# Kernel tuning notes

Hardware: AMD Instinct MI355X
Metric: run time of the kernel (lower is better)

## Reference

```python
import jax, jax.numpy as jnp
import numpy as np

# Fixed MANO structural constants (from MANO_RIGHT.pkl)
PARENTS = np.array([-1, 0, 1, 2, 0, 4, 5, 0, 7, 8, 0, 10, 11, 0, 13, 14])
FINGERTIP = np.array([745, 333, 444, 555, 672])
REMAP = np.array([0, 13, 14, 15, 16, 1, 2, 3, 17, 4, 5, 6, 18, 10, 11, 12, 19, 7, 8, 9, 20])
NV, NJ, NB, NP = 778, 16, 10, 135  # verts, joints, shape betas, pose-basis dim


def setup_inputs() -> dict:
    key = jax.random.key(0)
    ks = jax.random.split(key, 9)
    B = 8192
    beta = jax.random.normal(ks[0], (B, NB), jnp.float32)
    pose = jax.random.normal(ks[1], (B, NJ - 1, 3), jnp.float32) * 0.3
    rvec = jax.random.normal(ks[2], (B, 3), jnp.float32) * 0.3
    tvec = jax.random.normal(ks[3], (B, 3), jnp.float32)
    V = jax.random.normal(ks[4], (NV, 3), jnp.float32) * 0.1          # v_template
    S = jax.random.normal(ks[5], (NV, 3, NB), jnp.float32) * 0.01     # shapedirs
    P = jax.random.normal(ks[6], (NP, NV * 3), jnp.float32) * 0.01    # posedirs (reshaped, transposed)
    J_reg = jax.random.uniform(ks[7], (NJ, NV), jnp.float32)
    J_reg = J_reg / jnp.sum(J_reg, axis=-1, keepdims=True)
    W = jax.random.uniform(ks[8], (NV, NJ), jnp.float32)
    W = W / jnp.sum(W, axis=-1, keepdims=True)                        # skinning weights
    return {"beta": beta, "pose": pose, "rvec": rvec, "tvec": tvec,
            "V": V, "S": S, "P": P, "J_reg": J_reg, "W": W}


def _rodrigues(r):
    # r: [..., 3] axis-angle -> [..., 3, 3] rotation matrices
    sq = jnp.sum(r * r, axis=-1, keepdims=True)
    angle = jnp.sqrt(sq + 1e-8)
    axis = r / angle
    cos = jnp.cos(angle)[..., None]
    sin = jnp.sin(angle)[..., None]
    x, y, z = axis[..., 0], axis[..., 1], axis[..., 2]
    zeros = jnp.zeros_like(x)
    K = jnp.stack([zeros, -z, y, z, zeros, -x, -y, x, zeros], axis=-1)
    K = K.reshape(r.shape[:-1] + (3, 3))
    outer = axis[..., :, None] * axis[..., None, :]
    eye = jnp.eye(3, dtype=r.dtype)
    return cos * eye + (1.0 - cos) * outer + sin * K


def reference(beta, pose, rvec, tvec, V, S, P, J_reg, W):
    B = beta.shape[0]
    dtype = beta.dtype
    full_pose = jnp.concatenate([rvec[:, None, :], pose], axis=1)          # [B,16,3]
    # shape blendshapes
    v_shaped = V + jnp.einsum('bl,vkl->bvk', beta, S)                      # [B,778,3]
    Jrest = jnp.einsum('jv,bvk->bjk', J_reg, v_shaped)                     # [B,16,3]
    # pose blendshapes
    rot = _rodrigues(full_pose)                                            # [B,16,3,3]
    pose_feat = (rot[:, 1:] - jnp.eye(3, dtype=dtype)).reshape(B, NP)      # [B,135]
    v_posed = v_shaped + jnp.matmul(pose_feat, P).reshape(B, NV, 3)        # [B,778,3]
    # rigid transforms along the kinematic chain
    rel = Jrest.at[:, 1:].add(-Jrest[:, PARENTS[1:]])                      # parent-relative joint offsets
    T = jnp.zeros((B, NJ, 4, 4), dtype=dtype)
    T = T.at[..., :3, :3].set(rot).at[..., :3, 3].set(rel).at[..., 3, 3].set(1.0)
    chain = [T[:, 0]]
    for i in range(1, NJ):
        chain.append(jnp.matmul(chain[int(PARENTS[i])], T[:, i]))
    A = jnp.stack(chain, axis=1)                                           # [B,16,4,4] world transforms
    posed_joints = A[..., :3, 3]                                           # [B,16,3]
    # relative-to-rest transforms: A_rel = A - pad(A @ [Jrest;0])
    corr = jnp.einsum('bjmn,bjn->bjm', A[..., :3, :3], Jrest)
    A_rel = A.at[..., :3, 3].add(-corr)
    # linear blend skinning
    Tv = jnp.einsum('vj,bjmn->bvmn', W, A_rel)                             # [B,778,4,4]
    verts = jnp.einsum('bvmn,bvn->bvm', Tv[..., :3, :3], v_posed) + Tv[..., :3, 3]
    # 16 joints + 5 fingertips, remapped to 21 joints
    joints = jnp.concatenate([posed_joints, verts[:, FINGERTIP]], axis=1)[:, REMAP]
    verts = verts + tvec[:, None, :]
    joints = joints + tvec[:, None, :]
    return verts, joints
```

## Files before the change

kernel.cpp:

```cpp
#include <hip/hip_runtime.h>
#include <hip/hip_bf16.h>

typedef __attribute__((ext_vector_type(8))) short short8v;
typedef __attribute__((ext_vector_type(4))) float float4v;

#define BATCH 8192
#define NVERT 778
#define NJOINT 16
#define NPOSE 135
#define KEXT  160
#define NVT   52

#define WSB_JS    0u
#define WSB_PFX   4096u
#define WSB_A     (WSB_PFX  + 2621440u)
#define WSB_PTXF  (WSB_A    + 6291456u)
#define WSB_WF    (WSB_PTXF + 798720u)
#define WSB_ATF   (WSB_WF   + 53248u)

__global__ __launch_bounds__(256) void js_kernel(
    const float* __restrict__ S, const float* __restrict__ V,
    const float* __restrict__ J_reg, float* __restrict__ wsJS)
{
    int o = blockIdx.x * 4 + (threadIdx.x >> 6);
    int lane = threadIdx.x & 63;
    float s = 0.f;
    if (o < 480) {
        int j = o / 30, k = (o / 10) % 3, l = o % 10;
        for (int v = lane; v < NVERT; v += 64)
            s += J_reg[j * NVERT + v] * S[v * 30 + k * 10 + l];
    } else if (o < 528) {
        int o2 = o - 480;
        int j = o2 / 3, k = o2 % 3;
        for (int v = lane; v < NVERT; v += 64)
            s += J_reg[j * NVERT + v] * V[v * 3 + k];
    }
#pragma unroll
    for (int m = 32; m >= 1; m >>= 1) s += __shfl_xor(s, m, 64);
    if (lane == 0 && o < 528) wsJS[o] = s;
}

__device__ __forceinline__ void rodrigues(float x, float y, float z, float R[9])
{
    float sq = x * x + y * y + z * z;
    float angle = sqrtf(sq + 1e-8f);
    float inv = 1.0f / angle;
    float ax = x * inv, ay = y * inv, az = z * inv;
    float c = cosf(angle), s = sinf(angle);
    float ic = 1.0f - c;
    R[0] = c + ic * ax * ax;      R[1] = ic * ax * ay - s * az; R[2] = ic * ax * az + s * ay;
    R[3] = ic * ax * ay + s * az; R[4] = c + ic * ay * ay;      R[5] = ic * ay * az - s * ax;
    R[6] = ic * ax * az - s * ay; R[7] = ic * ay * az + s * ax; R[8] = c + ic * az * az;
}

__device__ __forceinline__ void writeATF(
    __hip_bfloat16* __restrict__ ATF, int b, int i,
    const float R[9], const float t[3], const float J[3], const float tv[3])
{
    int bt = b >> 4;
    int lane32 = ((i >> 3) << 4) + (b & 15);
    size_t base = (((size_t)bt * 12) * 32 + lane32) * 8 + (i & 7);
    float vals[12];
#pragma unroll
    for (int m = 0; m < 3; ++m) {
        vals[m * 4 + 0] = R[m * 3 + 0];
        vals[m * 4 + 1] = R[m * 3 + 1];
        vals[m * 4 + 2] = R[m * 3 + 2];
        vals[m * 4 + 3] = t[m] + tv[m] - (R[m * 3 + 0] * J[0] + R[m * 3 + 1] * J[1] + R[m * 3 + 2] * J[2]);
    }
#pragma unroll
    for (int mn = 0; mn < 12; ++mn)
        ATF[base + (size_t)mn * 256] = __float2bfloat16(vals[mn]);
}

__global__ __launch_bounds__(256) void buildchain_kernel(
    const float* __restrict__ S, const float* __restrict__ V,
    const float* __restrict__ P, const float* __restrict__ W,
    const float* __restrict__ beta, const float* __restrict__ pose,
    const float* __restrict__ rvec, const float* __restrict__ tvec,
    const float* __restrict__ wsJS,
    __hip_bfloat16* __restrict__ PtxF, __hip_bfloat16* __restrict__ WF,
    __hip_bfloat16* __restrict__ pfx, __hip_bfloat16* __restrict__ ATF,
    float* __restrict__ out_joints)
{
    if (blockIdx.x < 208) {
        int idx = blockIdx.x * 256 + threadIdx.x;
        if (idx < NVT * 3 * 5 * 64) {
            int vt = idx / 960;
            int rem = idx % 960;
            int k = rem / 320;
            int rem2 = rem % 320;
            int kc = rem2 / 64;
            int lane = rem2 % 64;
            int v = vt * 16 + (lane & 15);
            int kbase = kc * 32 + (lane >> 4) * 8;
            short8v out;
#pragma unroll
            for (int jj = 0; jj < 8; ++jj) {
                int kk = kbase + jj;
                float val = 0.f;
                if (v < NVERT) {
                    if (kk < NPOSE)            val = P[(size_t)kk * (NVERT * 3) + v * 3 + k];
                    else if (kk < NPOSE + 10)  val = S[v * 30 + k * 10 + (kk - NPOSE)];
                    else if (kk == NPOSE + 10) val = V[v * 3 + k];
                }
                __hip_bfloat16 h = __float2bfloat16(val);
                out[jj] = *reinterpret_cast<short*>(&h);
            }
            ((short8v*)PtxF)[idx] = out;
        } else if (idx < NVT * 3 * 5 * 64 + NVT * 64) {
            int t = idx - NVT * 3 * 5 * 64;
            int vt = t / 64, lane = t % 64;
            int v = vt * 16 + (lane & 15);
            int jbase = (lane >> 4) * 8;
            short8v out;
#pragma unroll
            for (int jj = 0; jj < 8; ++jj) {
                int j = jbase + jj;
                float val = (j < 16 && v < NVERT) ? W[v * 16 + j] : 0.f;
                __hip_bfloat16 h = __float2bfloat16(val);
                out[jj] = *reinterpret_cast<short*>(&h);
            }
            ((short8v*)WF)[t] = out;
        }
        return;
    }

    int t = (blockIdx.x - 208) * 256 + threadIdx.x;
    int c = t >> 13;
    int b = t & (BATCH - 1);
    if (c >= 5) return;

    const int INVMAP[16] = {0, 5, 6, 7, 9, 10, 11, 17, 18, 19, 13, 14, 15, 1, 2, 3};

    float bt[10];
#pragma unroll
    for (int l = 0; l < 10; ++l) bt[l] = beta[b * 10 + l];

    float Jr0[3], Jrc[3][3];
#pragma unroll
    for (int k = 0; k < 3; ++k) {
        float s = wsJS[480 + k];
#pragma unroll
        for (int l = 0; l < 10; ++l) s += wsJS[k * 10 + l] * bt[l];
        Jr0[k] = s;
    }
#pragma unroll
    for (int sI = 0; sI < 3; ++sI) {
        int j = 3 * c + 1 + sI;
#pragma unroll
        for (int k = 0; k < 3; ++k) {
            float s = wsJS[480 + j * 3 + k];
#pragma unroll
            for (int l = 0; l < 10; ++l) s += wsJS[(j * 3 + k) * 10 + l] * bt[l];
            Jrc[sI][k] = s;
        }
    }

    float tv[3] = {tvec[b * 3 + 0], tvec[b * 3 + 1], tvec[b * 3 + 2]};

    float R0[9];
    rodrigues(rvec[b * 3 + 0], rvec[b * 3 + 1], rvec[b * 3 + 2], R0);
    float t0[3] = {Jr0[0], Jr0[1], Jr0[2]};

    __hip_bfloat16* pfb = pfx + (size_t)b * KEXT;
    float* jout = out_joints + (size_t)b * 63;

    if (c == 0) {
#pragma unroll
        for (int l = 0; l < 10; ++l) pfb[NPOSE + l] = __float2bfloat16(bt[l]);
        pfb[NPOSE + 10] = __float2bfloat16(1.0f);
#pragma unroll
        for (int l = NPOSE + 11; l < KEXT; ++l) pfb[l] = __float2bfloat16(0.0f);

#pragma unroll
        for (int k = 0; k < 3; ++k) jout[INVMAP[0] * 3 + k] = t0[k] + tv[k];
        writeATF(ATF, b, 0, R0, t0, Jr0, tv);
    }

    float Rc[9], tc[3], prevJ[3];
#pragma unroll
    for (int q = 0; q < 9; ++q) Rc[q] = R0[q];
#pragma unroll
    for (int k = 0; k < 3; ++k) { tc[k] = t0[k]; prevJ[k] = Jr0[k]; }

#pragma unroll
    for (int s = 0; s < 3; ++s) {
        int i = 3 * c + 1 + s;
        float Ri[9];
        rodrigues(pose[b * 45 + (i - 1) * 3 + 0],
                  pose[b * 45 + (i - 1) * 3 + 1],
                  pose[b * 45 + (i - 1) * 3 + 2], Ri);
#pragma unroll
        for (int mn = 0; mn < 9; ++mn)
            pfb[(i - 1) * 9 + mn] =
                __float2bfloat16(Ri[mn] - ((mn == 0 || mn == 4 || mn == 8) ? 1.0f : 0.0f));

        float rel[3];
#pragma unroll
        for (int k = 0; k < 3; ++k) rel[k] = Jrc[s][k] - prevJ[k];

        float Rn[9], tn[3];
#pragma unroll
        for (int m = 0; m < 3; ++m) {
#pragma unroll
            for (int n = 0; n < 3; ++n)
                Rn[m * 3 + n] = Rc[m * 3 + 0] * Ri[0 + n] + Rc[m * 3 + 1] * Ri[3 + n] + Rc[m * 3 + 2] * Ri[6 + n];
            tn[m] = Rc[m * 3 + 0] * rel[0] + Rc[m * 3 + 1] * rel[1] + Rc[m * 3 + 2] * rel[2] + tc[m];
        }
#pragma unroll
        for (int q = 0; q < 9; ++q) Rc[q] = Rn[q];
#pragma unroll
        for (int k = 0; k < 3; ++k) { tc[k] = tn[k]; prevJ[k] = Jrc[s][k]; }

#pragma unroll
        for (int k = 0; k < 3; ++k) jout[INVMAP[i] * 3 + k] = tc[k] + tv[k];

        writeATF(ATF, b, i, Rc, tc, Jrc[s], tv);
    }
}

__device__ __forceinline__ void stage_tile(
    const __hip_bfloat16* __restrict__ PtxF,
    const __hip_bfloat16* __restrict__ WF,
    int vt, short* dst, int wave, int lane)
{
#pragma unroll
    for (int c = 0; c < 4; ++c) {
        int g = wave * 4 + c;
        const char* src = (g < 15)
            ? (const char*)PtxF + ((size_t)vt * 15 + g) * 1024
            : (const char*)WF + (size_t)vt * 1024;
        src += lane * 16;
        char* d = (char*)dst + g * 1024;
        __builtin_amdgcn_global_load_lds(
            (const __attribute__((address_space(1))) void*)src,
            (__attribute__((address_space(3))) void*)d,
            16, 0, 0);
    }
}

__global__ __launch_bounds__(256, 3) void verts_kernel(
    const __hip_bfloat16* __restrict__ pfx,
    const __hip_bfloat16* __restrict__ PtxF,
    const __hip_bfloat16* __restrict__ WF,
    const __hip_bfloat16* __restrict__ ATF,
    float* __restrict__ out_verts, float* __restrict__ out_joints)
{
    __shared__ __align__(16) short Bs[2][16 * 64 * 8];

    int tid = threadIdx.x;
    int lane = tid & 63;
    int wave = tid >> 6;
    int l15 = lane & 15;
    int lg  = lane >> 4;

    int bt = blockIdx.x * 4 + wave;
    int b0 = bt * 16;
    int vg = blockIdx.y;

    int start = (vg == 0) ? 0 : 7 + (vg - 1) * 6;
    int count = (vg == 0) ? 7 : 6;

    short8v hA[5];
#pragma unroll
    for (int kc = 0; kc < 5; ++kc)
        hA[kc] = *(const short8v*)(pfx + (size_t)(b0 + l15) * KEXT + kc * 32 + lg * 8);

    short8v tA[12];
#pragma unroll
    for (int mn = 0; mn < 12; ++mn)
        tA[mn] = *(const short8v*)(ATF + (((size_t)bt * 12 + mn) * 32 + (lane & 31)) * 8);

    stage_tile(PtxF, WF, start, &Bs[0][0], wave, lane);
    asm volatile("s_waitcnt vmcnt(0)" ::: "memory");
    __builtin_amdgcn_s_barrier();
    __builtin_amdgcn_sched_barrier(0);

    for (int i = 0; i < count; ++i) {
        int vt = start + i;
        const short* cur = &Bs[i & 1][0];

        if (i + 1 < count)
            stage_tile(PtxF, WF, vt + 1, &Bs[(i + 1) & 1][0], wave, lane);
        __builtin_amdgcn_sched_barrier(0);

        float4v hacc[3], Tacc[12];
#pragma unroll
        for (int k = 0; k < 3; ++k) hacc[k] = (float4v){0.f, 0.f, 0.f, 0.f};
#pragma unroll
        for (int mn = 0; mn < 12; ++mn) Tacc[mn] = (float4v){0.f, 0.f, 0.f, 0.f};

#pragma unroll
        for (int f = 0; f < 15; ++f) {
            short8v hB = *(const short8v*)(cur + f * 512 + lane * 8);
            hacc[f / 5] = __builtin_amdgcn_mfma_f32_16x16x32_bf16(
                hA[f % 5], hB, hacc[f / 5], 0, 0, 0);
        }
        short8v wf = *(const short8v*)(cur + 15 * 512 + lane * 8);
#pragma unroll
        for (int mn = 0; mn < 12; ++mn)
            Tacc[mn] = __builtin_amdgcn_mfma_f32_16x16x32_bf16(
                tA[mn], wf, Tacc[mn], 0, 0, 0);

        int v = vt * 16 + l15;
        int dest = (v == 745) ? 4 : (v == 333) ? 8 : (v == 444) ? 12 :
                   (v == 555) ? 16 : (v == 672) ? 20 : -1;

        if (v < NVERT) {
#pragma unroll
            for (int r = 0; r < 4; ++r) {
                float h0 = hacc[0][r], h1 = hacc[1][r], h2 = hacc[2][r];
                float e0 = Tacc[0][r] * h0 + Tacc[1][r] * h1 + Tacc[2][r]  * h2 + Tacc[3][r];
                float e1 = Tacc[4][r] * h0 + Tacc[5][r] * h1 + Tacc[6][r]  * h2 + Tacc[7][r];
                float e2 = Tacc[8][r] * h0 + Tacc[9][r] * h1 + Tacc[10][r] * h2 + Tacc[11][r];
                int b = b0 + lg * 4 + r;
                size_t idx = ((size_t)b * NVERT + v) * 3;
                out_verts[idx + 0] = e0;
                out_verts[idx + 1] = e1;
                out_verts[idx + 2] = e2;
                if (dest >= 0) {
                    size_t jidx = (size_t)b * 63 + dest * 3;
                    out_joints[jidx + 0] = e0;
                    out_joints[jidx + 1] = e1;
                    out_joints[jidx + 2] = e2;
                }
            }
        }

        if (i + 1 < count) {
            asm volatile("s_waitcnt vmcnt(4)" ::: "memory");
            __builtin_amdgcn_s_barrier();
            __builtin_amdgcn_sched_barrier(0);
        }
    }
}

extern "C" void kernel_launch(void* const* d_in, const int* in_sizes, int n_in,
                              void* d_out, int out_size, void* d_ws, size_t ws_size,
                              hipStream_t stream)
{
    const float* beta  = (const float*)d_in[0];
    const float* pose  = (const float*)d_in[1];
    const float* rvec  = (const float*)d_in[2];
    const float* tvec  = (const float*)d_in[3];
    const float* V     = (const float*)d_in[4];
    const float* S     = (const float*)d_in[5];
    const float* P     = (const float*)d_in[6];
    const float* J_reg = (const float*)d_in[7];
    const float* W     = (const float*)d_in[8];

    float* out    = (float*)d_out;
    float* verts  = out;
    float* joints = out + (size_t)BATCH * NVERT * 3;

    char* wsb = (char*)d_ws;
    float*          wsJS = (float*)(wsb + WSB_JS);
    __hip_bfloat16* pfx  = (__hip_bfloat16*)(wsb + WSB_PFX);
    __hip_bfloat16* PtxF = (__hip_bfloat16*)(wsb + WSB_PTXF);
    __hip_bfloat16* WFp  = (__hip_bfloat16*)(wsb + WSB_WF);
    __hip_bfloat16* ATF  = (__hip_bfloat16*)(wsb + WSB_ATF);

    hipLaunchKernelGGL(js_kernel, dim3(132), dim3(256), 0, stream,
                       S, V, J_reg, wsJS);
    hipLaunchKernelGGL(buildchain_kernel, dim3(368), dim3(256), 0, stream,
                       S, V, P, W, beta, pose, rvec, tvec, wsJS,
                       PtxF, WFp, pfx, ATF, joints);
    hipLaunchKernelGGL(verts_kernel, dim3(128, 8), dim3(256), 0, stream,
                       pfx, PtxF, WFp, ATF, verts, joints);
}
```

Baseline: 48.74 us.

## Move weight-matrix prep into joint-regressor kernel and reload transforms per tile

The constant-weight repacking (posedirs/shapedirs/template and skinning weights into bf16 fragments) moves from the chain kernel into the first kernel, next to the joint-regressor reduction. The chain kernel now runs only the per-batch kinematic chain with a smaller grid. In the verts kernel, the 12 transform fragments are reloaded from global memory on every vertex tile instead of being held in registers for the whole loop, which lowers register pressure. The cost is repeated global or cache loads per tile.

```diff
diff --git a/kernel.cpp b/kernel.cpp
--- a/kernel.cpp
+++ b/kernel.cpp
@@ -18,26 +18,72 @@
 #define WSB_WF    (WSB_PTXF + 798720u)
 #define WSB_ATF   (WSB_WF   + 53248u)
 
-__global__ __launch_bounds__(256) void js_kernel(
+__global__ __launch_bounds__(256) void prep_kernel(
     const float* __restrict__ S, const float* __restrict__ V,
-    const float* __restrict__ J_reg, float* __restrict__ wsJS)
-{
-    int o = blockIdx.x * 4 + (threadIdx.x >> 6);
-    int lane = threadIdx.x & 63;
-    float s = 0.f;
-    if (o < 480) {
-        int j = o / 30, k = (o / 10) % 3, l = o % 10;
-        for (int v = lane; v < NVERT; v += 64)
-            s += J_reg[j * NVERT + v] * S[v * 30 + k * 10 + l];
-    } else if (o < 528) {
-        int o2 = o - 480;
-        int j = o2 / 3, k = o2 % 3;
-        for (int v = lane; v < NVERT; v += 64)
-            s += J_reg[j * NVERT + v] * V[v * 3 + k];
-    }
-#pragma unroll
-    for (int m = 32; m >= 1; m >>= 1) s += __shfl_xor(s, m, 64);
-    if (lane == 0 && o < 528) wsJS[o] = s;
+    const float* __restrict__ J_reg, const float* __restrict__ P,
+    const float* __restrict__ W,
+    float* __restrict__ wsJS, __hip_bfloat16* __restrict__ PtxF,
+    __hip_bfloat16* __restrict__ WF)
+{
+    if (blockIdx.x < 132) {
+        int o = blockIdx.x * 4 + (threadIdx.x >> 6);
+        int lane = threadIdx.x & 63;
+        float s = 0.f;
+        if (o < 480) {
+            int j = o / 30, k = (o / 10) % 3, l = o % 10;
+            for (int v = lane; v < NVERT; v += 64)
+                s += J_reg[j * NVERT + v] * S[v * 30 + k * 10 + l];
+        } else if (o < 528) {
+            int o2 = o - 480;
+            int j = o2 / 3, k = o2 % 3;
+            for (int v = lane; v < NVERT; v += 64)
+                s += J_reg[j * NVERT + v] * V[v * 3 + k];
+        }
+#pragma unroll
+        for (int m = 32; m >= 1; m >>= 1) s += __shfl_xor(s, m, 64);
+        if (lane == 0 && o < 528) wsJS[o] = s;
+        return;
+    }
+
+    int idx = (blockIdx.x - 132) * 256 + threadIdx.x;
+    if (idx < NVT * 3 * 5 * 64) {
+        int vt = idx / 960;
+        int rem = idx % 960;
+        int k = rem / 320;
+        int rem2 = rem % 320;
+        int kc = rem2 / 64;
+        int lane = rem2 % 64;
+        int v = vt * 16 + (lane & 15);
+        int kbase = kc * 32 + (lane >> 4) * 8;
+        short8v out;
+#pragma unroll
+        for (int jj = 0; jj < 8; ++jj) {
+            int kk = kbase + jj;
+            float val = 0.f;
+            if (v < NVERT) {
+                if (kk < NPOSE)            val = P[(size_t)kk * (NVERT * 3) + v * 3 + k];
+                else if (kk < NPOSE + 10)  val = S[v * 30 + k * 10 + (kk - NPOSE)];
+                else if (kk == NPOSE + 10) val = V[v * 3 + k];
+            }
+            __hip_bfloat16 h = __float2bfloat16(val);
+            out[jj] = *reinterpret_cast<short*>(&h);
+        }
+        ((short8v*)PtxF)[idx] = out;
+    } else if (idx < NVT * 3 * 5 * 64 + NVT * 64) {
+        int t = idx - NVT * 3 * 5 * 64;
+        int vt = t / 64, lane = t % 64;
+        int v = vt * 16 + (lane & 15);
+        int jbase = (lane >> 4) * 8;
+        short8v out;
+#pragma unroll
+        for (int jj = 0; jj < 8; ++jj) {
+            int j = jbase + jj;
+            float val = (j < 16 && v < NVERT) ? W[v * 16 + j] : 0.f;
+            __hip_bfloat16 h = __float2bfloat16(val);
+            out[jj] = *reinterpret_cast<short*>(&h);
+        }
+        ((short8v*)WF)[t] = out;
+    }
 }
 
 __device__ __forceinline__ void rodrigues(float x, float y, float z, float R[9])
@@ -73,60 +119,13 @@
         ATF[base + (size_t)mn * 256] = __float2bfloat16(vals[mn]);
 }
 
-__global__ __launch_bounds__(256) void buildchain_kernel(
-    const float* __restrict__ S, const float* __restrict__ V,
-    const float* __restrict__ P, const float* __restrict__ W,
+__global__ __launch_bounds__(256) void chain_kernel(
     const float* __restrict__ beta, const float* __restrict__ pose,
     const float* __restrict__ rvec, const float* __restrict__ tvec,
-    const float* __restrict__ wsJS,
-    __hip_bfloat16* __restrict__ PtxF, __hip_bfloat16* __restrict__ WF,
-    __hip_bfloat16* __restrict__ pfx, __hip_bfloat16* __restrict__ ATF,
-    float* __restrict__ out_joints)
-{
-    if (blockIdx.x < 208) {
-        int idx = blockIdx.x * 256 + threadIdx.x;
-        if (idx < NVT * 3 * 5 * 64) {
-            int vt = idx / 960;
-            int rem = idx % 960;
-            int k = rem / 320;
-            int rem2 = rem % 320;
-            int kc = rem2 / 64;
-            int lane = rem2 % 64;
-            int v = vt * 16 + (lane & 15);
-            int kbase = kc * 32 + (lane >> 4) * 8;
-            short8v out;
-#pragma unroll
-            for (int jj = 0; jj < 8; ++jj) {
-                int kk = kbase + jj;
-                float val = 0.f;
-                if (v < NVERT) {
-                    if (kk < NPOSE)            val = P[(size_t)kk * (NVERT * 3) + v * 3 + k];
-                    else if (kk < NPOSE + 10)  val = S[v * 30 + k * 10 + (kk - NPOSE)];
-                    else if (kk == NPOSE + 10) val = V[v * 3 + k];
-                }
-                __hip_bfloat16 h = __float2bfloat16(val);
-                out[jj] = *reinterpret_cast<short*>(&h);
-            }
-            ((short8v*)PtxF)[idx] = out;
-        } else if (idx < NVT * 3 * 5 * 64 + NVT * 64) {
-            int t = idx - NVT * 3 * 5 * 64;
-            int vt = t / 64, lane = t % 64;
-            int v = vt * 16 + (lane & 15);
-            int jbase = (lane >> 4) * 8;
-            short8v out;
-#pragma unroll
-            for (int jj = 0; jj < 8; ++jj) {
-                int j = jbase + jj;
-                float val = (j < 16 && v < NVERT) ? W[v * 16 + j] : 0.f;
-                __hip_bfloat16 h = __float2bfloat16(val);
-                out[jj] = *reinterpret_cast<short*>(&h);
-            }
-            ((short8v*)WF)[t] = out;
-        }
-        return;
-    }
-
-    int t = (blockIdx.x - 208) * 256 + threadIdx.x;
+    const float* __restrict__ wsJS, __hip_bfloat16* __restrict__ pfx,
+    __hip_bfloat16* __restrict__ ATF, float* __restrict__ out_joints)
+{
+    int t = blockIdx.x * 256 + threadIdx.x;
     int c = t >> 13;
     int b = t & (BATCH - 1);
     if (c >= 5) return;
@@ -267,10 +266,7 @@
     for (int kc = 0; kc < 5; ++kc)
         hA[kc] = *(const short8v*)(pfx + (size_t)(b0 + l15) * KEXT + kc * 32 + lg * 8);
 
-    short8v tA[12];
-#pragma unroll
-    for (int mn = 0; mn < 12; ++mn)
-        tA[mn] = *(const short8v*)(ATF + (((size_t)bt * 12 + mn) * 32 + (lane & 31)) * 8);
+    const short8v* atf_base = (const short8v*)(ATF + (((size_t)bt * 12) * 32 + (lane & 31)) * 8);
 
     stage_tile(PtxF, WF, start, &Bs[0][0], wave, lane);
     asm volatile("s_waitcnt vmcnt(0)" ::: "memory");
@@ -285,19 +281,25 @@
             stage_tile(PtxF, WF, vt + 1, &Bs[(i + 1) & 1][0], wave, lane);
         __builtin_amdgcn_sched_barrier(0);
 
-        float4v hacc[3], Tacc[12];
+        short8v wf = *(const short8v*)(cur + 15 * 512 + lane * 8);
+        short8v tA[12];
+#pragma unroll
+        for (int mn = 0; mn < 12; ++mn)
+            tA[mn] = atf_base[(size_t)mn * 32];
+
+        float4v hacc[3];
 #pragma unroll
         for (int k = 0; k < 3; ++k) hacc[k] = (float4v){0.f, 0.f, 0.f, 0.f};
-#pragma unroll
-        for (int mn = 0; mn < 12; ++mn) Tacc[mn] = (float4v){0.f, 0.f, 0.f, 0.f};
-
 #pragma unroll
         for (int f = 0; f < 15; ++f) {
             short8v hB = *(const short8v*)(cur + f * 512 + lane * 8);
             hacc[f / 5] = __builtin_amdgcn_mfma_f32_16x16x32_bf16(
                 hA[f % 5], hB, hacc[f / 5], 0, 0, 0);
         }
-        short8v wf = *(const short8v*)(cur + 15 * 512 + lane * 8);
+
+        float4v Tacc[12];
+#pragma unroll
+        for (int mn = 0; mn < 12; ++mn) Tacc[mn] = (float4v){0.f, 0.f, 0.f, 0.f};
 #pragma unroll
         for (int mn = 0; mn < 12; ++mn)
             Tacc[mn] = __builtin_amdgcn_mfma_f32_16x16x32_bf16(
@@ -361,11 +363,10 @@
     __hip_bfloat16* WFp  = (__hip_bfloat16*)(wsb + WSB_WF);
     __hip_bfloat16* ATF  = (__hip_bfloat16*)(wsb + WSB_ATF);
 
-    hipLaunchKernelGGL(js_kernel, dim3(132), dim3(256), 0, stream,
-                       S, V, J_reg, wsJS);
-    hipLaunchKernelGGL(buildchain_kernel, dim3(368), dim3(256), 0, stream,
-                       S, V, P, W, beta, pose, rvec, tvec, wsJS,
-                       PtxF, WFp, pfx, ATF, joints);
+    hipLaunchKernelGGL(prep_kernel, dim3(340), dim3(256), 0, stream,
+                       S, V, J_reg, P, W, wsJS, PtxF, WFp);
+    hipLaunchKernelGGL(chain_kernel, dim3(160), dim3(256), 0, stream,
+                       beta, pose, rvec, tvec, wsJS, pfx, ATF, joints);
     hipLaunchKernelGGL(verts_kernel, dim3(128, 8), dim3(256), 0, stream,
                        pfx, PtxF, WFp, ATF, verts, joints);
 }
```

New measurement: 49.34 us. Within noise of the previous version (+1.2%).
